# Performance work log

Measured on AMD Instinct MI355X. Metric: run time of the kernel, lower is better.

## Reference

```python
import jax, jax.numpy as jnp
import numpy as np

TOPK = 32  # init kwarg topk=32, method='softmax'


def setup_inputs() -> dict:
    key = jax.random.key(0)
    k1, k2 = jax.random.split(key)
    X1 = jax.random.normal(k1, (8192, 64), dtype=jnp.float32)
    X2 = jax.random.normal(k2, (8192, 64), dtype=jnp.float32)
    return {"X1": X1, "X2": X2}


def reference(X1, X2):
    # pairwise Euclidean distance via the matmul expansion (same math as torch.cdist p=2)
    sq = (
        jnp.sum(X1 * X1, axis=-1)[:, None]
        + jnp.sum(X2 * X2, axis=-1)[None, :]
        - 2.0 * (X1 @ X2.T)
    )  # [N1, N2]
    neg_dist = -jnp.sqrt(jnp.maximum(sq, 0.0))
    # top-k along dim=1, softmax over the k selected values
    val, idx = jax.lax.top_k(neg_dist, TOPK)          # [N1, K]
    score = jax.nn.softmax(val, axis=1)               # [N1, K]
    # scatter scores back into a dense zero matrix
    rows = jnp.arange(neg_dist.shape[0])[:, None]     # [N1, 1]
    out = jnp.zeros_like(neg_dist).at[rows, idx].set(score)
    return out, score
```

## Files before the change

kernel.cpp:

```cpp
#include <hip/hip_runtime.h>
#include <math.h>
#include <float.h>
#include <limits.h>

#define N 8192
#define D 64
#define TOPK 32
#define TILE 128
#define CAP 1024
#define SLOT 32
#define CAPR 768
#define MARGIN 0.75f

typedef _Float16 f16x8 __attribute__((ext_vector_type(8)));
typedef _Float16 f16x4v __attribute__((ext_vector_type(4)));
typedef __attribute__((ext_vector_type(4))) float f32x4;

__device__ __forceinline__ unsigned ford(float f) {
    unsigned u = __float_as_uint(f);
    return u ^ ((u & 0x80000000u) ? 0xFFFFFFFFu : 0x80000000u);
}
__device__ __forceinline__ float finv(unsigned u) {
    unsigned b = (u & 0x80000000u) ? (u ^ 0x80000000u) : ~u;
    return __uint_as_float(b);
}

__global__ __launch_bounds__(256) void prep_kernel(
    const float* __restrict__ X1, const float* __restrict__ X2,
    float* __restrict__ nrm,
    _Float16* __restrict__ X1f, _Float16* __restrict__ X2f)
{
    int id = blockIdx.x * blockDim.x + threadIdx.x;
    if (id >= 2 * N) return;
    const float* X = (id < N) ? X1 : X2;
    _Float16* H = (id < N) ? X1f : X2f;
    int r = (id < N) ? id : id - N;
    const float4* p = (const float4*)(X + (size_t)r * D);
    f16x4v* ph = (f16x4v*)(H + (size_t)r * D);
    float s = 0.f;
#pragma unroll
    for (int q = 0; q < D / 4; ++q) {
        float4 v = p[q];
        s += v.x * v.x + v.y * v.y + v.z * v.z + v.w * v.w;
        f16x4v h;
        h[0] = (_Float16)v.x; h[1] = (_Float16)v.y;
        h[2] = (_Float16)v.z; h[3] = (_Float16)v.w;
        ph[q] = h;
    }
    nrm[id] = s;
}

#define MFMA16F(a, b, c) __builtin_amdgcn_mfma_f32_16x16x32_f16((a), (b), (c), 0, 0, 0)

__device__ __forceinline__ void stage_tile(
    const _Float16* __restrict__ gsrc, _Float16* __restrict__ lds, int t)
{
    const f16x8* g = (const f16x8*)gsrc;
#pragma unroll
    for (int it = 0; it < 4; ++it) {
        int idx = it * 256 + t;
        int row = idx >> 3;
        int co  = (idx & 7) << 3;
        int sw  = co ^ ((row & 7) << 3);
        *(f16x8*)&lds[row * 64 + sw] = g[idx];
    }
}

__device__ __forceinline__ void mfma_core_lds(
    const _Float16* __restrict__ Asm, const _Float16* __restrict__ Bsm,
    int wr, int wc, int lane, f32x4 acc[4][4])
{
    const int l15 = lane & 15;
    const int lg8 = (lane >> 4) * 8;

    f16x8 ah[4][2];
#pragma unroll
    for (int mt = 0; mt < 4; ++mt) {
        int row = wr * 64 + mt * 16 + l15;
        int sw0 = (lg8)      ^ ((row & 7) << 3);
        int sw1 = (32 + lg8) ^ ((row & 7) << 3);
        ah[mt][0] = *(const f16x8*)&Asm[row * 64 + sw0];
        ah[mt][1] = *(const f16x8*)&Asm[row * 64 + sw1];
    }
#pragma unroll
    for (int nt = 0; nt < 4; ++nt) {
        int row = wc * 64 + nt * 16 + l15;
        int sw0 = (lg8)      ^ ((row & 7) << 3);
        int sw1 = (32 + lg8) ^ ((row & 7) << 3);
        f16x8 b0 = *(const f16x8*)&Bsm[row * 64 + sw0];
        f16x8 b1 = *(const f16x8*)&Bsm[row * 64 + sw1];
#pragma unroll
        for (int mt = 0; mt < 4; ++mt) {
            acc[mt][nt] = MFMA16F(ah[mt][0], b0, acc[mt][nt]);
            acc[mt][nt] = MFMA16F(ah[mt][1], b1, acc[mt][nt]);
        }
    }
}

__global__ __launch_bounds__(256) void mfma_tmax_kernel(
    const _Float16* __restrict__ X1f, const _Float16* __restrict__ X2f,
    const float* __restrict__ nrm, float* __restrict__ tmax)
{
    __shared__ _Float16 Asm[TILE * D];
    __shared__ _Float16 Bsm[TILE * D];
    __shared__ float red[128][2];

    const int t = threadIdx.x;
    const int lane = t & 63, w = t >> 6;
    const int wr = w >> 1, wc = w & 1;
    const int row0 = blockIdx.y * TILE, col0 = blockIdx.x * TILE;
    const int l15 = lane & 15, lg = lane >> 4;

    stage_tile(X1f + (size_t)row0 * D, Asm, t);
    stage_tile(X2f + (size_t)col0 * D, Bsm, t);
    __syncthreads();

    f32x4 acc[4][4];
#pragma unroll
    for (int mt = 0; mt < 4; ++mt)
#pragma unroll
        for (int nt = 0; nt < 4; ++nt)
            acc[mt][nt] = (f32x4){0.f, 0.f, 0.f, 0.f};

    mfma_core_lds(Asm, Bsm, wr, wc, lane, acc);

    float nb[4];
#pragma unroll
    for (int nt = 0; nt < 4; ++nt) nb[nt] = nrm[N + col0 + wc * 64 + nt * 16 + l15];

    float rmax[4][4];
#pragma unroll
    for (int mt = 0; mt < 4; ++mt) {
#pragma unroll
        for (int reg = 0; reg < 4; ++reg) {
            float na = nrm[row0 + wr * 64 + mt * 16 + lg * 4 + reg];
            float m = -FLT_MAX;
#pragma unroll
            for (int nt = 0; nt < 4; ++nt) {
                float v = -fmaxf(na + nb[nt] - 2.0f * acc[mt][nt][reg], 0.f);
                m = fmaxf(m, v);
            }
            rmax[mt][reg] = m;
        }
    }
#pragma unroll
    for (int off = 1; off < 16; off <<= 1)
#pragma unroll
        for (int mt = 0; mt < 4; ++mt)
#pragma unroll
            for (int reg = 0; reg < 4; ++reg)
                rmax[mt][reg] = fmaxf(rmax[mt][reg], __shfl_xor(rmax[mt][reg], off));

    if (l15 == 0) {
#pragma unroll
        for (int mt = 0; mt < 4; ++mt)
#pragma unroll
            for (int reg = 0; reg < 4; ++reg)
                red[wr * 64 + mt * 16 + lg * 4 + reg][wc] = rmax[mt][reg];
    }
    __syncthreads();
    if (t < 128)
        tmax[(size_t)(row0 + t) * 64 + blockIdx.x] = fmaxf(red[t][0], red[t][1]);
}

__global__ __launch_bounds__(256) void thr_kernel(
    const float* __restrict__ tmax, float* __restrict__ thr)
{
    const int t = threadIdx.x;
    const int w = t >> 6;
    const int lane = t & 63;
    const int r = blockIdx.x * 4 + w;

    float tm = tmax[(size_t)r * 64 + lane];
    unsigned km = ford(tm);
    int rk = 0;
#pragma unroll
    for (int l = 0; l < 64; ++l) {
        unsigned o = __shfl(km, l);
        rk += (o > km || (o == km && l < lane)) ? 1 : 0;
    }
    unsigned long long bm = __ballot(rk == 31);
    float tv = __shfl(tm, __ffsll(bm) - 1);
    if (lane == 0) thr[r] = tv - MARGIN;
}

__global__ __launch_bounds__(256) void mfma_cand_kernel(
    const _Float16* __restrict__ X1f, const _Float16* __restrict__ X2f,
    const float* __restrict__ nrm, const float* __restrict__ thr,
    float* __restrict__ out, unsigned short* __restrict__ cand,
    int* __restrict__ cnt)
{
    __shared__ _Float16 Asm[TILE * D];
    __shared__ _Float16 Bsm[TILE * D];
    __shared__ unsigned short lbuf[128][SLOT];
    __shared__ int lcnt[128];

    const int t = threadIdx.x;
    const int lane = t & 63, w = t >> 6;
    const int wr = w >> 1, wc = w & 1;
    const int row0 = blockIdx.y * TILE, col0 = blockIdx.x * TILE;
    const int l15 = lane & 15, lg = lane >> 4;

    if (t < 128) lcnt[t] = 0;
    stage_tile(X1f + (size_t)row0 * D, Asm, t);
    stage_tile(X2f + (size_t)col0 * D, Bsm, t);

    const float4 zz = make_float4(0.f, 0.f, 0.f, 0.f);
#pragma unroll
    for (int p = 0; p < 16; ++p) {
        int lin = p * 256 + t;
        int rr = lin >> 5;
        int c4 = (lin & 31) << 2;
        *(float4*)(out + (size_t)(row0 + rr) * N + col0 + c4) = zz;
    }
    __syncthreads();

    f32x4 acc[4][4];
#pragma unroll
    for (int mt = 0; mt < 4; ++mt)
#pragma unroll
        for (int nt = 0; nt < 4; ++nt)
            acc[mt][nt] = (f32x4){0.f, 0.f, 0.f, 0.f};

    mfma_core_lds(Asm, Bsm, wr, wc, lane, acc);

    float nb[4];
#pragma unroll
    for (int nt = 0; nt < 4; ++nt) nb[nt] = nrm[N + col0 + wc * 64 + nt * 16 + l15];

#pragma unroll
    for (int mt = 0; mt < 4; ++mt) {
#pragma unroll
        for (int reg = 0; reg < 4; ++reg) {
            int lrow = wr * 64 + mt * 16 + lg * 4 + reg;
            float na = nrm[row0 + lrow];
            float th = thr[row0 + lrow];
#pragma unroll
            for (int nt = 0; nt < 4; ++nt) {
                float v = -fmaxf(na + nb[nt] - 2.0f * acc[mt][nt][reg], 0.f);
                if (v >= th) {
                    int p0 = atomicAdd(&lcnt[lrow], 1);
                    if (p0 < SLOT)
                        lbuf[lrow][p0] = (unsigned short)(wc * 64 + nt * 16 + l15);
                }
            }
        }
    }
    __syncthreads();

    if (t < 128) {
        int c = lcnt[t];
        size_t sidx = (size_t)(row0 + t) * 64 + blockIdx.x;
        cnt[sidx] = c;
        unsigned short* cg = cand + sidx * SLOT;
        int m = min(c, SLOT);
        for (int j = 0; j < m; ++j) cg[j] = lbuf[t][j];
    }
}

__global__ __launch_bounds__(256) void exact_topk_kernel(
    const float* __restrict__ X1, const float* __restrict__ X2,
    const float* __restrict__ nrm,
    const unsigned short* __restrict__ cand, const int* __restrict__ cnt,
    float* __restrict__ out, float* __restrict__ score_out)
{
    __shared__ float x1r[4][D];
    __shared__ unsigned short lst[4][CAPR];
    __shared__ unsigned long long kl[4][CAPR];

    const int t = threadIdx.x;
    const int w = t >> 6;
    const int lane = t & 63;
    const int r = blockIdx.x * 4 + w;

    x1r[w][lane] = X1[(size_t)r * D + lane];

    int c = cnt[(size_t)r * 64 + lane];
    int eff = (c > SLOT) ? 128 : c;
    int pre = eff;
#pragma unroll
    for (int o = 1; o < 64; o <<= 1) {
        int pv = __shfl_up(pre, o);
        if (lane >= o) pre += pv;
    }
    int off0 = pre - eff;
    int M = __shfl(pre, 63);
    if (M > CAPR) M = CAPR;

    const unsigned short* cg = cand + ((size_t)r * 64 + lane) * SLOT;
    for (int j = 0; j < eff; ++j) {
        int pos = off0 + j;
        if (pos < CAPR) {
            int colloc = (c > SLOT) ? j : (int)cg[j];
            lst[w][pos] = (unsigned short)(lane * 128 + colloc);
        }
    }
    __builtin_amdgcn_s_waitcnt(0xC07F);

    float na = nrm[r];
    for (int q = lane; q < M; q += 64) {
        int col = lst[w][q];
        const float4* xr = (const float4*)(X2 + (size_t)col * D);
        float dot = 0.f;
#pragma unroll
        for (int i = 0; i < D / 4; ++i) {
            float4 xv = xr[i];
            dot += x1r[w][4 * i + 0] * xv.x + x1r[w][4 * i + 1] * xv.y
                 + x1r[w][4 * i + 2] * xv.z + x1r[w][4 * i + 3] * xv.w;
        }
        float v = -fmaxf(na + nrm[N + col] - 2.0f * dot, 0.f);
        kl[w][q] = ((unsigned long long)ford(v) << 32) | (unsigned)(8191 - col);
    }
    __builtin_amdgcn_s_waitcnt(0xC07F);

    unsigned long long mykey = 0ull;
    for (int it = 0; it < TOPK; ++it) {
        unsigned long long b = 0ull; int bp = 0;
        for (int q = lane; q < M; q += 64) {
            unsigned long long kk = kl[w][q];
            if (kk > b) { b = kk; bp = q; }
        }
        for (int off = 32; off > 0; off >>= 1) {
            unsigned long long ob = __shfl_down(b, off);
            int op = __shfl_down(bp, off);
            if (ob > b) { b = ob; bp = op; }
        }
        unsigned long long b0 = __shfl(b, 0);
        int bp0 = __shfl(bp, 0);
        if (lane == it) { mykey = b0; kl[w][bp0] = 0ull; }
    }

    float myv = -FLT_MAX; int myj = 0;
    if (lane < TOPK && mykey != 0ull) {
        float sv = finv((unsigned)(mykey >> 32));
        myv = -sqrtf(-sv);
        myj = 8191 - (int)(mykey & 0xFFFFFFFFu);
    }
    float Mx = __shfl(myv, 0);
    float e = (lane < TOPK && mykey != 0ull) ? expf(myv - Mx) : 0.f;
    float Z = e;
    for (int off = 32; off > 0; off >>= 1) Z += __shfl_xor(Z, off);
    float s = e / Z;
    if (lane < TOPK && mykey != 0ull) {
        score_out[(size_t)r * TOPK + lane] = s;
        out[(size_t)r * N + myj] = s;
    }
}

__global__ __launch_bounds__(256) void norms_kernel(
    const float* __restrict__ X1, const float* __restrict__ X2,
    float* __restrict__ nrm)
{
    int id = blockIdx.x * blockDim.x + threadIdx.x;
    if (id >= 2 * N) return;
    const float* X = (id < N) ? X1 : X2;
    int r = (id < N) ? id : id - N;
    const float4* p = (const float4*)(X + (size_t)r * D);
    float s = 0.f;
#pragma unroll
    for (int q = 0; q < D / 4; ++q) {
        float4 v = p[q];
        s += v.x * v.x + v.y * v.y + v.z * v.z + v.w * v.w;
    }
    nrm[id] = s;
}

__global__ __launch_bounds__(256, 2) void dist_kernel(
    const float* __restrict__ X1, const float* __restrict__ X2,
    const float* __restrict__ nrm, float* __restrict__ out,
    float* __restrict__ tmax, int have_tmax)
{
    __shared__ float As[D * TILE];
    __shared__ float Bs[D * TILE];

    const int t = threadIdx.x;
    const int row0 = blockIdx.y * TILE;
    const int col0 = blockIdx.x * TILE;

#pragma unroll
    for (int p = 0; p < 8; ++p) {
        int lin = p * 256 + t;
        int r   = lin >> 4;
        int d4  = (lin & 15) << 2;
        int g   = (d4 >> 2) & 7;
        int cb  = r ^ (g << 3);
        float4 a = *(const float4*)(X1 + (size_t)(row0 + r) * D + d4);
        As[(d4 + 0) * TILE + cb] = a.x;
        As[(d4 + 1) * TILE + cb] = a.y;
        As[(d4 + 2) * TILE + cb] = a.z;
        As[(d4 + 3) * TILE + cb] = a.w;
        float4 b = *(const float4*)(X2 + (size_t)(col0 + r) * D + d4);
        Bs[(d4 + 0) * TILE + cb] = b.x;
        Bs[(d4 + 1) * TILE + cb] = b.y;
        Bs[(d4 + 2) * TILE + cb] = b.z;
        Bs[(d4 + 3) * TILE + cb] = b.w;
    }
    __syncthreads();

    const int tx = t & 15;
    const int ty = t >> 4;
    float acc[8][8] = {};

#pragma unroll 8
    for (int k = 0; k < D; ++k) {
        int gk  = (k >> 2) & 7;
        int ab  = k * TILE + ((ty ^ gk) << 3);
        int bb0 = k * TILE + ((4 * tx) ^ (gk << 3));
        float4 a0 = *(const float4*)&As[ab];
        float4 a1 = *(const float4*)&As[ab + 4];
        float4 b0 = *(const float4*)&Bs[bb0];
        float4 b1 = *(const float4*)&Bs[bb0 + 64];
        float av[8] = {a0.x, a0.y, a0.z, a0.w, a1.x, a1.y, a1.z, a1.w};
        float bv[8] = {b0.x, b0.y, b0.z, b0.w, b1.x, b1.y, b1.z, b1.w};
#pragma unroll
        for (int i = 0; i < 8; ++i)
#pragma unroll
            for (int j = 0; j < 8; ++j)
                acc[i][j] += av[i] * bv[j];
    }

    float na[8], nb[8];
#pragma unroll
    for (int i = 0; i < 8; ++i) na[i] = nrm[row0 + 8 * ty + i];
#pragma unroll
    for (int q = 0; q < 4; ++q) {
        nb[q]     = nrm[N + col0 + 4 * tx + q];
        nb[4 + q] = nrm[N + col0 + 64 + 4 * tx + q];
    }

    float rmax[8];
#pragma unroll
    for (int i = 0; i < 8; ++i) rmax[i] = -FLT_MAX;

#pragma unroll
    for (int i = 0; i < 8; ++i) {
        float* po = out + (size_t)(row0 + 8 * ty + i) * N + col0 + 4 * tx;
        float4 o0, o1;
        float* f0 = (float*)&o0;
        float* f1 = (float*)&o1;
#pragma unroll
        for (int q = 0; q < 4; ++q) {
            float s0 = na[i] + nb[q] - 2.0f * acc[i][q];
            f0[q] = -fmaxf(s0, 0.0f);
            float s1 = na[i] + nb[4 + q] - 2.0f * acc[i][4 + q];
            f1[q] = -fmaxf(s1, 0.0f);
            rmax[i] = fmaxf(rmax[i], fmaxf(f0[q], f1[q]));
        }
        *(float4*)po        = o0;
        *(float4*)(po + 64) = o1;
    }

    if (have_tmax) {
#pragma unroll
        for (int i = 0; i < 8; ++i) {
            float mv = rmax[i];
            mv = fmaxf(mv, __shfl_down(mv, 8, 16));
            mv = fmaxf(mv, __shfl_down(mv, 4, 16));
            mv = fmaxf(mv, __shfl_down(mv, 2, 16));
            mv = fmaxf(mv, __shfl_down(mv, 1, 16));
            if (tx == 0)
                tmax[(size_t)(row0 + 8 * ty + i) * 64 + blockIdx.x] = mv;
        }
    }
}

__global__ __launch_bounds__(256) void topk_kernel(
    float* __restrict__ out, float* __restrict__ score_out,
    const float* __restrict__ tmax, int have_tmax)
{
    __shared__ unsigned long long candl[4][CAP];
    __shared__ int scnt[4];

    const int t    = threadIdx.x;
    const int w    = t >> 6;
    const int lane = t & 63;
    const int r    = blockIdx.x * 4 + w;
    float* row = out + (size_t)r * N;
    const float4* row4 = (const float4*)row;

    float thr;
    float lm = -FLT_MAX;
    if (have_tmax) {
        float tm = tmax[(size_t)r * 64 + lane];
        unsigned km = ford(tm);
        int rk = 0;
#pragma unroll
        for (int l = 0; l < 64; ++l) {
            unsigned o = __shfl(km, l);
            rk += (o > km || (o == km && l < lane)) ? 1 : 0;
        }
        unsigned long long bm = __ballot(rk == 31);
        thr = __shfl(tm, __ffsll(bm) - 1);
    } else {
#pragma unroll 8
        for (int c = 0; c < 32; ++c) {
            float4 x = row4[c * 64 + lane];
            lm = fmaxf(lm, fmaxf(fmaxf(x.x, x.y), fmaxf(x.z, x.w)));
        }
        thr = lm;
        for (int off = 32; off > 0; off >>= 1)
            thr = fminf(thr, __shfl_xor(thr, off));
    }

    for (int attempt = 0; ; ++attempt) {
        if (lane == 0) scnt[w] = 0;
        __builtin_amdgcn_s_waitcnt(0xC07F);
        for (int c = 0; c < 32; ++c) {
            float4 x = row4[c * 64 + lane];
            float vs[4] = {x.x, x.y, x.z, x.w};
#pragma unroll
            for (int q = 0; q < 4; ++q) {
                float v = vs[q];
                lm = fmaxf(lm, v);
                if (v >= thr) {
                    int p = atomicAdd(&scnt[w], 1);
                    if (p < CAP) {
                        unsigned long long key =
                            ((unsigned long long)ford(v) << 32) |
                            (unsigned)(8191 - (4 * (c * 64 + lane) + q));
                        candl[w][p] = key;
                    }
                }
            }
        }
        __builtin_amdgcn_s_waitcnt(0xC07F);
        if (scnt[w] <= CAP || attempt == 1) break;
        unsigned kml = ford(lm);
        int rk2 = 0;
#pragma unroll
        for (int l = 0; l < 64; ++l) {
            unsigned o = __shfl(kml, l);
            rk2 += (o < kml || (o == kml && l < lane)) ? 1 : 0;
        }
        unsigned long long bm2 = __ballot(rk2 == 15);
        float t2 = __shfl(lm, __ffsll(bm2) - 1);
        thr = fmaxf(thr, t2);
    }
    const int n = min(scnt[w], CAP);

    unsigned long long mykey = 0ull;
    for (int it = 0; it < TOPK; ++it) {
        unsigned long long b = 0ull; int bp = 0;
        for (int q = lane; q < n; q += 64) {
            unsigned long long kk = candl[w][q];
            if (kk > b) { b = kk; bp = q; }
        }
        for (int off = 32; off > 0; off >>= 1) {
            unsigned long long ob = __shfl_down(b, off);
            int op = __shfl_down(bp, off);
            if (ob > b) { b = ob; bp = op; }
        }
        unsigned long long b0 = __shfl(b, 0);
        int bp0 = __shfl(bp, 0);
        if (lane == it) { mykey = b0; candl[w][bp0] = 0ull; }
    }

    float myv = 0.f; int myj = 0;
    if (lane < TOPK) {
        float sv = finv((unsigned)(mykey >> 32));
        myv = -sqrtf(-sv);
        myj = 8191 - (int)(mykey & 0xFFFFFFFFu);
    }
    float Mx = __shfl(myv, 0);
    float e = (lane < TOPK) ? expf(myv - Mx) : 0.f;
    float Z = e;
    for (int off = 32; off > 0; off >>= 1) Z += __shfl_xor(Z, off);
    float s = e / Z;
    if (lane < TOPK) score_out[(size_t)r * TOPK + lane] = s;

    const float4 zz = make_float4(0.f, 0.f, 0.f, 0.f);
#pragma unroll 8
    for (int c = 0; c < 32; ++c) ((float4*)row)[c * 64 + lane] = zz;
    __builtin_amdgcn_s_waitcnt(0x0F70);
    if (lane < TOPK) row[myj] = s;
}

extern "C" void kernel_launch(void* const* d_in, const int* in_sizes, int n_in,
                              void* d_out, int out_size, void* d_ws, size_t ws_size,
                              hipStream_t stream)
{
    const float* X1 = (const float*)d_in[0];
    const float* X2 = (const float*)d_in[1];
    float* out = (float*)d_out;
    float* score = out + (size_t)N * N;

    char* base = (char*)d_ws;
    float* nrm  = (float*)base;
    float* tmax = nrm + 2 * N;
    float* thrv = tmax + (size_t)N * 64;
    int*   cnt  = (int*)(thrv + N);
    _Float16* X1f = (_Float16*)(cnt + (size_t)N * 64);
    _Float16* X2f = X1f + (size_t)N * D;
    unsigned short* cand = (unsigned short*)(X2f + (size_t)N * D);

    size_t need_new = (size_t)(2 * N + (size_t)N * 64 + N) * sizeof(float)
                    + (size_t)N * 64 * sizeof(int)
                    + 2 * (size_t)N * D * sizeof(_Float16)
                    + (size_t)N * 64 * SLOT * sizeof(unsigned short);
    size_t need_old = (size_t)(2 * N + (size_t)N * 64) * sizeof(float);

    if (ws_size >= need_new) {
        prep_kernel<<<(2 * N + 255) / 256, 256, 0, stream>>>(X1, X2, nrm, X1f, X2f);
        dim3 grid(N / TILE, N / TILE);
        mfma_tmax_kernel<<<grid, 256, 0, stream>>>(X1f, X2f, nrm, tmax);
        thr_kernel<<<N / 4, 256, 0, stream>>>(tmax, thrv);
        mfma_cand_kernel<<<grid, 256, 0, stream>>>(X1f, X2f, nrm, thrv, out, cand, cnt);
        exact_topk_kernel<<<N / 4, 256, 0, stream>>>(X1, X2, nrm, cand, cnt, out, score);
    } else {
        float* tmax_f = nrm + 2 * N;
        int have_tmax = (ws_size >= need_old) ? 1 : 0;
        norms_kernel<<<(2 * N + 255) / 256, 256, 0, stream>>>(X1, X2, nrm);
        dim3 grid(N / TILE, N / TILE);
        dist_kernel<<<grid, 256, 0, stream>>>(X1, X2, nrm, out, tmax_f, have_tmax);
        topk_kernel<<<N / 4, 256, 0, stream>>>(out, score, tmax_f, have_tmax);
    }
}
```

Measured before the change: 443.4 us.

## Estimate top-k threshold from a strided sample of columns instead of full pass

The threshold pre-pass now computes distances against only every eighth X2 row (1024 sampled columns) rather than all 8192. Each 16-column group keeps its own maximum, so every row still gets 64 tile maxima, and the existing rank-based threshold kernel runs unchanged. This removes most of the MFMA work in the first distance pass. In exchange the threshold is looser, so more candidates may pass into the later exact stage, and the per-row candidate capacity CAPR is raised from 768 to 1024 to absorb that.

```diff
diff --git a/kernel.cpp b/kernel.cpp
--- a/kernel.cpp
+++ b/kernel.cpp
@@ -9,8 +9,10 @@
 #define TILE 128
 #define CAP 1024
 #define SLOT 32
-#define CAPR 768
+#define CAPR 1024
 #define MARGIN 0.75f
+#define SSTRIDE 8
+#define MS 1024
 
 typedef _Float16 f16x8 __attribute__((ext_vector_type(8)));
 typedef _Float16 f16x4v __attribute__((ext_vector_type(4)));
@@ -66,6 +68,20 @@
     }
 }
 
+__device__ __forceinline__ void stage_tile_strided(
+    const _Float16* __restrict__ X2f, int srow0, _Float16* __restrict__ lds, int t)
+{
+#pragma unroll
+    for (int it = 0; it < 4; ++it) {
+        int idx = it * 256 + t;
+        int row = idx >> 3;
+        int co  = (idx & 7) << 3;
+        int sw  = co ^ ((row & 7) << 3);
+        *(f16x8*)&lds[row * 64 + sw] =
+            *(const f16x8*)(X2f + (size_t)(srow0 + row) * SSTRIDE * D + co);
+    }
+}
+
 __device__ __forceinline__ void mfma_core_lds(
     const _Float16* __restrict__ Asm, const _Float16* __restrict__ Bsm,
     int wr, int wc, int lane, f32x4 acc[4][4])
@@ -97,22 +113,22 @@
     }
 }
 
-__global__ __launch_bounds__(256) void mfma_tmax_kernel(
+__global__ __launch_bounds__(256) void mfma_stmax_kernel(
     const _Float16* __restrict__ X1f, const _Float16* __restrict__ X2f,
     const float* __restrict__ nrm, float* __restrict__ tmax)
 {
     __shared__ _Float16 Asm[TILE * D];
     __shared__ _Float16 Bsm[TILE * D];
-    __shared__ float red[128][2];
 
     const int t = threadIdx.x;
     const int lane = t & 63, w = t >> 6;
     const int wr = w >> 1, wc = w & 1;
-    const int row0 = blockIdx.y * TILE, col0 = blockIdx.x * TILE;
+    const int row0 = blockIdx.y * TILE;
+    const int scol0 = blockIdx.x * TILE;
     const int l15 = lane & 15, lg = lane >> 4;
 
     stage_tile(X1f + (size_t)row0 * D, Asm, t);
-    stage_tile(X2f + (size_t)col0 * D, Bsm, t);
+    stage_tile_strided(X2f, scol0, Bsm, t);
     __syncthreads();
 
     f32x4 acc[4][4];
@@ -126,41 +142,36 @@
 
     float nb[4];
 #pragma unroll
-    for (int nt = 0; nt < 4; ++nt) nb[nt] = nrm[N + col0 + wc * 64 + nt * 16 + l15];
-
-    float rmax[4][4];
+    for (int nt = 0; nt < 4; ++nt)
+        nb[nt] = nrm[N + (size_t)(scol0 + wc * 64 + nt * 16 + l15) * SSTRIDE];
+
 #pragma unroll
     for (int mt = 0; mt < 4; ++mt) {
+        float vm[4][4];
 #pragma unroll
         for (int reg = 0; reg < 4; ++reg) {
             float na = nrm[row0 + wr * 64 + mt * 16 + lg * 4 + reg];
-            float m = -FLT_MAX;
-#pragma unroll
-            for (int nt = 0; nt < 4; ++nt) {
-                float v = -fmaxf(na + nb[nt] - 2.0f * acc[mt][nt][reg], 0.f);
-                m = fmaxf(m, v);
+#pragma unroll
+            for (int nt = 0; nt < 4; ++nt)
+                vm[reg][nt] = -fmaxf(na + nb[nt] - 2.0f * acc[mt][nt][reg], 0.f);
+        }
+#pragma unroll
+        for (int off = 1; off < 16; off <<= 1)
+#pragma unroll
+            for (int reg = 0; reg < 4; ++reg)
+#pragma unroll
+                for (int nt = 0; nt < 4; ++nt)
+                    vm[reg][nt] = fmaxf(vm[reg][nt], __shfl_xor(vm[reg][nt], off));
+        if (l15 == 0) {
+#pragma unroll
+            for (int reg = 0; reg < 4; ++reg) {
+                size_t rowi = row0 + wr * 64 + mt * 16 + lg * 4 + reg;
+#pragma unroll
+                for (int nt = 0; nt < 4; ++nt)
+                    tmax[rowi * 64 + blockIdx.x * 8 + wc * 4 + nt] = vm[reg][nt];
             }
-            rmax[mt][reg] = m;
-        }
-    }
-#pragma unroll
-    for (int off = 1; off < 16; off <<= 1)
-#pragma unroll
-        for (int mt = 0; mt < 4; ++mt)
-#pragma unroll
-            for (int reg = 0; reg < 4; ++reg)
-                rmax[mt][reg] = fmaxf(rmax[mt][reg], __shfl_xor(rmax[mt][reg], off));
-
-    if (l15 == 0) {
-#pragma unroll
-        for (int mt = 0; mt < 4; ++mt)
-#pragma unroll
-            for (int reg = 0; reg < 4; ++reg)
-                red[wr * 64 + mt * 16 + lg * 4 + reg][wc] = rmax[mt][reg];
-    }
-    __syncthreads();
-    if (t < 128)
-        tmax[(size_t)(row0 + t) * 64 + blockIdx.x] = fmaxf(red[t][0], red[t][1]);
+        }
+    }
 }
 
 __global__ __launch_bounds__(256) void thr_kernel(
@@ -601,9 +612,10 @@
 
     if (ws_size >= need_new) {
         prep_kernel<<<(2 * N + 255) / 256, 256, 0, stream>>>(X1, X2, nrm, X1f, X2f);
+        dim3 sgrid(MS / TILE, N / TILE);
+        mfma_stmax_kernel<<<sgrid, 256, 0, stream>>>(X1f, X2f, nrm, tmax);
+        thr_kernel<<<N / 4, 256, 0, stream>>>(tmax, thrv);
         dim3 grid(N / TILE, N / TILE);
-        mfma_tmax_kernel<<<grid, 256, 0, stream>>>(X1f, X2f, nrm, tmax);
-        thr_kernel<<<N / 4, 256, 0, stream>>>(tmax, thrv);
         mfma_cand_kernel<<<grid, 256, 0, stream>>>(X1f, X2f, nrm, thrv, out, cand, cnt);
         exact_topk_kernel<<<N / 4, 256, 0, stream>>>(X1, X2, nrm, cand, cnt, out, score);
     } else {
```

After: 537.2 us. 1.21x slower.

## Store fp16 squared-distance matrix once and scan it instead of recomputing candidates

Applied to the files above, without the earlier changes.

The first MFMA pass now writes the full negated squared-distance matrix to workspace as fp16 and still records per-tile maxima. The second MFMA candidate pass is removed. A fused per-row kernel scans the fp16 row against the threshold, collects up to 256 candidates, recomputes exact fp32 distances, selects top-k, and zeroes and writes the output row. This trades a second GEMM plus compact candidate lists for a 128 MB fp16 write and read. It also drops the guard for missing keys and raises the margin, which risks overflowing the candidate cap.

```diff
diff --git a/kernel.cpp b/kernel.cpp
--- a/kernel.cpp
+++ b/kernel.cpp
@@ -8,9 +8,8 @@
 #define TOPK 32
 #define TILE 128
 #define CAP 1024
-#define SLOT 32
-#define CAPR 768
-#define MARGIN 0.75f
+#define CAP2 256
+#define MARGIN 1.0f
 
 typedef _Float16 f16x8 __attribute__((ext_vector_type(8)));
 typedef _Float16 f16x4v __attribute__((ext_vector_type(4)));
@@ -97,13 +96,16 @@
     }
 }
 
-__global__ __launch_bounds__(256) void mfma_tmax_kernel(
+__global__ __launch_bounds__(256) void mfma_s_kernel(
     const _Float16* __restrict__ X1f, const _Float16* __restrict__ X2f,
-    const float* __restrict__ nrm, float* __restrict__ tmax)
-{
-    __shared__ _Float16 Asm[TILE * D];
-    __shared__ _Float16 Bsm[TILE * D];
+    const float* __restrict__ nrm, _Float16* __restrict__ S,
+    float* __restrict__ tmax)
+{
+    __shared__ _Float16 smem[TILE * TILE];
     __shared__ float red[128][2];
+
+    _Float16* Asm = smem;
+    _Float16* Bsm = smem + TILE * D;
 
     const int t = threadIdx.x;
     const int lane = t & 63, w = t >> 6;
@@ -128,21 +130,37 @@
 #pragma unroll
     for (int nt = 0; nt < 4; ++nt) nb[nt] = nrm[N + col0 + wc * 64 + nt * 16 + l15];
 
+    __syncthreads();
+
     float rmax[4][4];
 #pragma unroll
     for (int mt = 0; mt < 4; ++mt) {
 #pragma unroll
         for (int reg = 0; reg < 4; ++reg) {
-            float na = nrm[row0 + wr * 64 + mt * 16 + lg * 4 + reg];
-            float m = -FLT_MAX;
+            int lrow = wr * 64 + mt * 16 + lg * 4 + reg;
+            float na = nrm[row0 + lrow];
+            float rm = -FLT_MAX;
 #pragma unroll
             for (int nt = 0; nt < 4; ++nt) {
                 float v = -fmaxf(na + nb[nt] - 2.0f * acc[mt][nt][reg], 0.f);
-                m = fmaxf(m, v);
+                _Float16 h = (_Float16)v;
+                smem[lrow * TILE + wc * 64 + nt * 16 + l15] = h;
+                rm = fmaxf(rm, (float)h);
             }
-            rmax[mt][reg] = m;
-        }
-    }
+            rmax[mt][reg] = rm;
+        }
+    }
+    __syncthreads();
+
+#pragma unroll
+    for (int it = 0; it < 8; ++it) {
+        int idx = it * 256 + t;
+        int row = idx >> 4;
+        int c8  = (idx & 15) << 3;
+        *(f16x8*)(S + (size_t)(row0 + row) * N + col0 + c8) =
+            *(const f16x8*)&smem[row * TILE + c8];
+    }
+
 #pragma unroll
     for (int off = 1; off < 16; off <<= 1)
 #pragma unroll
@@ -184,89 +202,16 @@
     if (lane == 0) thr[r] = tv - MARGIN;
 }
 
-__global__ __launch_bounds__(256) void mfma_cand_kernel(
-    const _Float16* __restrict__ X1f, const _Float16* __restrict__ X2f,
+__global__ __launch_bounds__(256) void fused_topk_kernel(
+    const float* __restrict__ X1, const float* __restrict__ X2,
     const float* __restrict__ nrm, const float* __restrict__ thr,
-    float* __restrict__ out, unsigned short* __restrict__ cand,
-    int* __restrict__ cnt)
-{
-    __shared__ _Float16 Asm[TILE * D];
-    __shared__ _Float16 Bsm[TILE * D];
-    __shared__ unsigned short lbuf[128][SLOT];
-    __shared__ int lcnt[128];
-
-    const int t = threadIdx.x;
-    const int lane = t & 63, w = t >> 6;
-    const int wr = w >> 1, wc = w & 1;
-    const int row0 = blockIdx.y * TILE, col0 = blockIdx.x * TILE;
-    const int l15 = lane & 15, lg = lane >> 4;
-
-    if (t < 128) lcnt[t] = 0;
-    stage_tile(X1f + (size_t)row0 * D, Asm, t);
-    stage_tile(X2f + (size_t)col0 * D, Bsm, t);
-
-    const float4 zz = make_float4(0.f, 0.f, 0.f, 0.f);
-#pragma unroll
-    for (int p = 0; p < 16; ++p) {
-        int lin = p * 256 + t;
-        int rr = lin >> 5;
-        int c4 = (lin & 31) << 2;
-        *(float4*)(out + (size_t)(row0 + rr) * N + col0 + c4) = zz;
-    }
-    __syncthreads();
-
-    f32x4 acc[4][4];
-#pragma unroll
-    for (int mt = 0; mt < 4; ++mt)
-#pragma unroll
-        for (int nt = 0; nt < 4; ++nt)
-            acc[mt][nt] = (f32x4){0.f, 0.f, 0.f, 0.f};
-
-    mfma_core_lds(Asm, Bsm, wr, wc, lane, acc);
-
-    float nb[4];
-#pragma unroll
-    for (int nt = 0; nt < 4; ++nt) nb[nt] = nrm[N + col0 + wc * 64 + nt * 16 + l15];
-
-#pragma unroll
-    for (int mt = 0; mt < 4; ++mt) {
-#pragma unroll
-        for (int reg = 0; reg < 4; ++reg) {
-            int lrow = wr * 64 + mt * 16 + lg * 4 + reg;
-            float na = nrm[row0 + lrow];
-            float th = thr[row0 + lrow];
-#pragma unroll
-            for (int nt = 0; nt < 4; ++nt) {
-                float v = -fmaxf(na + nb[nt] - 2.0f * acc[mt][nt][reg], 0.f);
-                if (v >= th) {
-                    int p0 = atomicAdd(&lcnt[lrow], 1);
-                    if (p0 < SLOT)
-                        lbuf[lrow][p0] = (unsigned short)(wc * 64 + nt * 16 + l15);
-                }
-            }
-        }
-    }
-    __syncthreads();
-
-    if (t < 128) {
-        int c = lcnt[t];
-        size_t sidx = (size_t)(row0 + t) * 64 + blockIdx.x;
-        cnt[sidx] = c;
-        unsigned short* cg = cand + sidx * SLOT;
-        int m = min(c, SLOT);
-        for (int j = 0; j < m; ++j) cg[j] = lbuf[t][j];
-    }
-}
-
-__global__ __launch_bounds__(256) void exact_topk_kernel(
-    const float* __restrict__ X1, const float* __restrict__ X2,
-    const float* __restrict__ nrm,
-    const unsigned short* __restrict__ cand, const int* __restrict__ cnt,
-    float* __restrict__ out, float* __restrict__ score_out)
+    const _Float16* __restrict__ S, float* __restrict__ out,
+    float* __restrict__ score_out)
 {
     __shared__ float x1r[4][D];
-    __shared__ unsigned short lst[4][CAPR];
-    __shared__ unsigned long long kl[4][CAPR];
+    __shared__ unsigned short lst[4][CAP2];
+    __shared__ unsigned long long kl[4][CAP2];
+    __shared__ int scnt[4];
 
     const int t = threadIdx.x;
     const int w = t >> 6;
@@ -274,31 +219,29 @@
     const int r = blockIdx.x * 4 + w;
 
     x1r[w][lane] = X1[(size_t)r * D + lane];
-
-    int c = cnt[(size_t)r * 64 + lane];
-    int eff = (c > SLOT) ? 128 : c;
-    int pre = eff;
-#pragma unroll
-    for (int o = 1; o < 64; o <<= 1) {
-        int pv = __shfl_up(pre, o);
-        if (lane >= o) pre += pv;
-    }
-    int off0 = pre - eff;
-    int M = __shfl(pre, 63);
-    if (M > CAPR) M = CAPR;
-
-    const unsigned short* cg = cand + ((size_t)r * 64 + lane) * SLOT;
-    for (int j = 0; j < eff; ++j) {
-        int pos = off0 + j;
-        if (pos < CAPR) {
-            int colloc = (c > SLOT) ? j : (int)cg[j];
-            lst[w][pos] = (unsigned short)(lane * 128 + colloc);
-        }
-    }
+    if (lane == 0) scnt[w] = 0;
+    const float th = thr[r];
     __builtin_amdgcn_s_waitcnt(0xC07F);
 
+    const _Float16* Sr = S + (size_t)r * N;
+#pragma unroll 4
+    for (int c = 0; c < 16; ++c) {
+        f16x8 h8 = *(const f16x8*)(Sr + (size_t)(c * 64 + lane) * 8);
+#pragma unroll
+        for (int q = 0; q < 8; ++q) {
+            float v = (float)h8[q];
+            if (v >= th) {
+                int p = atomicAdd(&scnt[w], 1);
+                if (p < CAP2)
+                    lst[w][p] = (unsigned short)((c * 64 + lane) * 8 + q);
+            }
+        }
+    }
+    __builtin_amdgcn_s_waitcnt(0xC07F);
+    const int n = min(scnt[w], CAP2);
+
     float na = nrm[r];
-    for (int q = lane; q < M; q += 64) {
+    for (int q = lane; q < n; q += 64) {
         int col = lst[w][q];
         const float4* xr = (const float4*)(X2 + (size_t)col * D);
         float dot = 0.f;
@@ -316,7 +259,7 @@
     unsigned long long mykey = 0ull;
     for (int it = 0; it < TOPK; ++it) {
         unsigned long long b = 0ull; int bp = 0;
-        for (int q = lane; q < M; q += 64) {
+        for (int q = lane; q < n; q += 64) {
             unsigned long long kk = kl[w][q];
             if (kk > b) { b = kk; bp = q; }
         }
@@ -330,21 +273,25 @@
         if (lane == it) { mykey = b0; kl[w][bp0] = 0ull; }
     }
 
-    float myv = -FLT_MAX; int myj = 0;
-    if (lane < TOPK && mykey != 0ull) {
+    float myv = 0.f; int myj = 0;
+    if (lane < TOPK) {
         float sv = finv((unsigned)(mykey >> 32));
         myv = -sqrtf(-sv);
         myj = 8191 - (int)(mykey & 0xFFFFFFFFu);
     }
     float Mx = __shfl(myv, 0);
-    float e = (lane < TOPK && mykey != 0ull) ? expf(myv - Mx) : 0.f;
+    float e = (lane < TOPK) ? expf(myv - Mx) : 0.f;
     float Z = e;
     for (int off = 32; off > 0; off >>= 1) Z += __shfl_xor(Z, off);
     float s = e / Z;
-    if (lane < TOPK && mykey != 0ull) {
-        score_out[(size_t)r * TOPK + lane] = s;
-        out[(size_t)r * N + myj] = s;
-    }
+    if (lane < TOPK) score_out[(size_t)r * TOPK + lane] = s;
+
+    float* row = out + (size_t)r * N;
+    const float4 zz = make_float4(0.f, 0.f, 0.f, 0.f);
+#pragma unroll 8
+    for (int c = 0; c < 32; ++c) ((float4*)row)[c * 64 + lane] = zz;
+    __builtin_amdgcn_s_waitcnt(0x0F70);
+    if (lane < TOPK) row[myj] = s;
 }
 
 __global__ __launch_bounds__(256) void norms_kernel(
@@ -588,24 +535,22 @@
     float* nrm  = (float*)base;
     float* tmax = nrm + 2 * N;
     float* thrv = tmax + (size_t)N * 64;
-    int*   cnt  = (int*)(thrv + N);
-    _Float16* X1f = (_Float16*)(cnt + (size_t)N * 64);
+    _Float16* X1f = (_Float16*)(thrv + N);
     _Float16* X2f = X1f + (size_t)N * D;
-    unsigned short* cand = (unsigned short*)(X2f + (size_t)N * D);
+    _Float16* S   = X2f + (size_t)N * D;
 
     size_t need_new = (size_t)(2 * N + (size_t)N * 64 + N) * sizeof(float)
-                    + (size_t)N * 64 * sizeof(int)
                     + 2 * (size_t)N * D * sizeof(_Float16)
-                    + (size_t)N * 64 * SLOT * sizeof(unsigned short);
+                    + (size_t)N * N * sizeof(_Float16);
     size_t need_old = (size_t)(2 * N + (size_t)N * 64) * sizeof(float);
 
     if (ws_size >= need_new) {
         prep_kernel<<<(2 * N + 255) / 256, 256, 0, stream>>>(X1, X2, nrm, X1f, X2f);
         dim3 grid(N / TILE, N / TILE);
-        mfma_tmax_kernel<<<grid, 256, 0, stream>>>(X1f, X2f, nrm, tmax);
+        mfma_s_kernel<<<grid, 256, 0, stream>>>(X1f, X2f, nrm, S, tmax);
         thr_kernel<<<N / 4, 256, 0, stream>>>(tmax, thrv);
-        mfma_cand_kernel<<<grid, 256, 0, stream>>>(X1f, X2f, nrm, thrv, out, cand, cnt);
-        exact_topk_kernel<<<N / 4, 256, 0, stream>>>(X1, X2, nrm, cand, cnt, out, score);
+        fused_topk_kernel<<<N / 4, 256, 0, stream>>>(
+            X1, X2, nrm, thrv, S, out, score);
     } else {
         float* tmax_f = nrm + 2 * N;
         int have_tmax = (ws_size >= need_old) ? 1 : 0;
```

New measurement: 382.7 us. 1.16x faster.
